# Optimization experiments

Measured on AMD Instinct MI355X. Metric: run time of the kernel, lower is better.

Reference implementation:

```python
import jax, jax.numpy as jnp
import numpy as np

B, NV, NDIRS, NRINGS, C, NF = 2, 30000, 8, 3, 16, 16


def setup_inputs() -> dict:
    key = jax.random.key(0)
    k1, k2, k3, k4, k5 = jax.random.split(key, 5)
    y = jax.random.normal(k1, (B, NV, NDIRS, C), dtype=jnp.float32)
    # sync_field: for each (batch, vertex, ring, dir) an index triple (b, v, d) into y
    v_idx = jax.random.randint(k2, (B, NV, NRINGS, NDIRS), 0, NV)
    d_idx = jax.random.randint(k3, (B, NV, NRINGS, NDIRS), 0, NDIRS)
    b_idx = jnp.broadcast_to(jnp.arange(B)[:, None, None, None], (B, NV, NRINGS, NDIRS))
    sync_field = jnp.stack([b_idx, v_idx, d_idx], axis=-1).astype(jnp.int32)
    kernel = jax.random.normal(k4, (NRINGS, NDIRS, C, NF), dtype=jnp.float32) * 0.05
    center_kernel = jax.random.normal(k5, (C, NF), dtype=jnp.float32) * 0.05
    bias = jnp.zeros((NF,), dtype=jnp.float32)
    return {"y": y, "sync_field": sync_field, "kernel": kernel,
            "center_kernel": center_kernel, "bias": bias}


def reference(y, sync_field, kernel, center_kernel, bias):
    b, nv, ndirs, c = y.shape
    nrings = kernel.shape[0]
    nf = kernel.shape[-1]
    # tf.gather_nd: index triples (batch, vertex, dir) -> channel vectors
    patches = y[sync_field[..., 0], sync_field[..., 1], sync_field[..., 2]]  # (b, nv, nrings, ndirs, c)
    patches = patches.reshape(b * nv, nrings, ndirs, c)
    # circular padding along direction axis: width becomes 2*ndirs-1
    patches = jnp.concatenate([patches, patches[:, :, :-1, :]], axis=2)
    # valid conv with (nrings, ndirs) kernel -> (b*nv, 1, ndirs, nf)
    out = jax.lax.conv_general_dilated(
        patches, kernel, window_strides=(1, 1), padding='VALID',
        dimension_numbers=('NHWC', 'HWIO', 'NHWC'))
    out = out.reshape(b, nv, ndirs, nf)
    out = out + jnp.einsum('bvdc,cf->bvdf', y, center_kernel) + bias
    out = jax.nn.relu(out)
    return jnp.max(out, axis=2)  # take_max over directions -> (b, nv, nf)
```

## Files before the change

kernel.cpp:

```cpp
#include <hip/hip_runtime.h>
#include <hip/hip_bf16.h>

static constexpr int kB = 2;
static constexpr int kNV = 30000;
static constexpr int kD = 8;
static constexpr int kR = 3;
static constexpr int kC = 16;
static constexpr int kF = 16;
static constexpr int NP = (kB * kNV) / 2;
static constexpr int S  = 4096;

typedef short short8  __attribute__((ext_vector_type(8)));
typedef float floatx4 __attribute__((ext_vector_type(4)));

static constexpr int CENT_OFS   = 1536;
static constexpr int BUF_STRIDE = 2560;

__device__ __forceinline__ unsigned pkbf16(float lo, float hi) {
    union { __hip_bfloat162 h; unsigned u; } cv;
    cv.h = __float22bfloat162_rn(make_float2(lo, hi));
    return cv.u;
}

__global__ __launch_bounds__(64, 4) void sgc_kernel(
    const float* __restrict__ y,
    const int*   __restrict__ sync_field,
    const float* __restrict__ kern,
    const float* __restrict__ ck,
    const float* __restrict__ bias,
    float*       __restrict__ out)
{
    __shared__ __align__(16) char smem[2 * BUF_STRIDE];

    const int lane = threadIdx.x;
    const int wid  = blockIdx.x;
    const int f    = lane & 15;
    const int q    = lane >> 4;
    const int mvtx = (lane >> 3) & 1;
    const int md   = lane & 7;
    const int eSub = lane >> 2;
    const int iq   = lane & 3;

    {
        const int buf = lane >> 5, z = lane & 31;
        const int ofs = buf * BUF_STRIDE + CENT_OFS + (z >> 1) * 64 + 32 + (z & 1) * 16;
        *(uint4*)(smem + ofs) = make_uint4(0u, 0u, 0u, 0u);
    }

    int aOfs[12];
    short8 bfrag[13];
#pragma unroll
    for (int kk = 0; kk < 12; ++kk) {
        const int g   = kk * 4 + q;
        const int dd  = (g * 43) >> 8;
        const int rem = g - dd * 6;
        const int r   = rem >> 1;
        const int ch  = rem & 1;
        const int rot = (md + dd) & 7;
        aOfs[kk] = ((mvtx * 3 + r) * 8 + rot) * 32 + ch * 16;
        const int be = ((r * 8 + dd) * 16 + ch * 8) * 16 + f;
        union { unsigned u[4]; short8 v; } t;
#pragma unroll
        for (int j = 0; j < 4; ++j)
            t.u[j] = pkbf16(kern[be + (2 * j) * 16], kern[be + (2 * j + 1) * 16]);
        bfrag[kk] = t.v;
    }
    {
        union { unsigned u[4]; short8 v; } t;
        if (q < 2) {
#pragma unroll
            for (int j = 0; j < 4; ++j)
                t.u[j] = pkbf16(ck[(q * 8 + 2 * j) * 16 + f],
                                ck[(q * 8 + 2 * j + 1) * 16 + f]);
        } else {
            t.u[0] = t.u[1] = t.u[2] = t.u[3] = 0u;
        }
        bfrag[12] = t.v;
    }
    const float biasv = bias[f];

    auto cl = [](int v) { return v < NP ? v : NP - 1; };

    int off[3];
    float4 A0, A1, A2, Ac, B0, B1, B2, Bc;

#define SF_PRE(cc) do { \
        const int base_ = (cc) * 48; \
        _Pragma("unroll") \
        for (int g_ = 0; g_ < 3; ++g_) { \
            const int* s_ = sync_field + (size_t)(base_ + g_ * 16 + eSub) * 3; \
            off[g_] = ((s_[0] * kNV + s_[1]) * kD + s_[2]) * 64 + iq * 16; \
        } \
    } while (0)

#define ISSUE_G(Rv, cc) do { \
        Rv##0 = *reinterpret_cast<const float4*>( \
                    reinterpret_cast<const char*>(y) + off[0]); \
        Rv##1 = *reinterpret_cast<const float4*>( \
                    reinterpret_cast<const char*>(y) + off[1]); \
        Rv##2 = *reinterpret_cast<const float4*>( \
                    reinterpret_cast<const char*>(y) + off[2]); \
        Rv##c = reinterpret_cast<const float4*>(y + (size_t)(cc) * 256)[lane]; \
    } while (0)

#define STAGE(Rv, bufbase) do { \
        const float4 g0_ = Rv##0, g1_ = Rv##1, g2_ = Rv##2, gc_ = Rv##c; \
        uint2 w_; \
        w_.x = pkbf16(g0_.x, g0_.y); w_.y = pkbf16(g0_.z, g0_.w); \
        *(uint2*)((bufbase) + 0 * 512 + lane * 8) = w_; \
        w_.x = pkbf16(g1_.x, g1_.y); w_.y = pkbf16(g1_.z, g1_.w); \
        *(uint2*)((bufbase) + 1 * 512 + lane * 8) = w_; \
        w_.x = pkbf16(g2_.x, g2_.y); w_.y = pkbf16(g2_.z, g2_.w); \
        *(uint2*)((bufbase) + 2 * 512 + lane * 8) = w_; \
        w_.x = pkbf16(gc_.x, gc_.y); w_.y = pkbf16(gc_.z, gc_.w); \
        *(uint2*)((bufbase) + CENT_OFS + eSub * 64 + iq * 8) = w_; \
    } while (0)

#define DRAIN do { \
        __asm__ __volatile__("" ::: "memory"); \
        __builtin_amdgcn_s_waitcnt(0xC07F);  \
        __asm__ __volatile__("" ::: "memory"); \
    } while (0)

#define COMPUTE_STORE(bufbase, pp) do { \
        floatx4 acc0 = { biasv, biasv, biasv, biasv }; \
        floatx4 acc1 = { 0.f, 0.f, 0.f, 0.f }; \
        _Pragma("unroll") \
        for (int kk_ = 0; kk_ < 12; kk_ += 2) { \
            const short8 a0_ = *(const short8*)((bufbase) + aOfs[kk_]); \
            const short8 a1_ = *(const short8*)((bufbase) + aOfs[kk_ + 1]); \
            acc0 = __builtin_amdgcn_mfma_f32_16x16x32_bf16(a0_, bfrag[kk_], acc0, 0, 0, 0); \
            acc1 = __builtin_amdgcn_mfma_f32_16x16x32_bf16(a1_, bfrag[kk_ + 1], acc1, 0, 0, 0); \
        } \
        { \
            const short8 ac_ = *(const short8*)((bufbase) + CENT_OFS \
                                                + (lane & 15) * 64 + q * 16); \
            acc0 = __builtin_amdgcn_mfma_f32_16x16x32_bf16(ac_, bfrag[12], acc0, 0, 0, 0); \
        } \
        float mx = fmaxf(fmaxf(acc0[0] + acc1[0], acc0[1] + acc1[1]), \
                         fmaxf(acc0[2] + acc1[2], acc0[3] + acc1[3])); \
        mx = fmaxf(mx, 0.0f); \
        mx = fmaxf(mx, __shfl_xor(mx, 16, 64)); \
        if (((lane >> 4) & 1) == 0) \
            out[(2 * (pp) + (lane >> 5)) * kF + f] = mx; \
    } while (0)

    int p = wid;
    SF_PRE(p);
    ISSUE_G(A, p);
    SF_PRE(cl(p + S));
    ISSUE_G(B, cl(p + S));
    SF_PRE(cl(p + 2 * S));
    STAGE(A, smem);
    ISSUE_G(A, cl(p + 2 * S));
    SF_PRE(cl(p + 3 * S));

    for (;;) {
        STAGE(B, smem + BUF_STRIDE);
        ISSUE_G(B, cl(p + 3 * S));
        SF_PRE(cl(p + 4 * S));
        DRAIN;
        COMPUTE_STORE(smem, p);
        p += S; if (p >= NP) break;

        STAGE(A, smem);
        ISSUE_G(A, cl(p + 3 * S));
        SF_PRE(cl(p + 4 * S));
        DRAIN;
        COMPUTE_STORE(smem + BUF_STRIDE, p);
        p += S; if (p >= NP) break;
    }

#undef SF_PRE
#undef ISSUE_G
#undef STAGE
#undef DRAIN
#undef COMPUTE_STORE
}

extern "C" void kernel_launch(void* const* d_in, const int* in_sizes, int n_in,
                              void* d_out, int out_size, void* d_ws, size_t ws_size,
                              hipStream_t stream) {
    const float* y    = reinterpret_cast<const float*>(d_in[0]);
    const int*   sf   = reinterpret_cast<const int*>(d_in[1]);
    const float* kern = reinterpret_cast<const float*>(d_in[2]);
    const float* ck   = reinterpret_cast<const float*>(d_in[3]);
    const float* bias = reinterpret_cast<const float*>(d_in[4]);
    float* out = reinterpret_cast<float*>(d_out);

    sgc_kernel<<<S, 64, 0, stream>>>(y, sf, kern, ck, bias, out);
}
```

Baseline: 131.2 us.

## Pre-convert y to a bf16 workspace table and gather bf16 in main kernel

Adds a prepass kernel that converts y from fp32 to bf16 into the workspace. The main kernel then gathers 8-byte bf16 vectors instead of 16-byte fp32 vectors, which halves the random-gather bytes and removes the per-element conversion before the LDS store. The grid size and launch bounds also change. The cost is an extra kernel launch plus a full read and write pass over y. An fp32 fallback path is kept for when the workspace is missing or too small.

```diff
diff --git a/kernel.cpp b/kernel.cpp
--- a/kernel.cpp
+++ b/kernel.cpp
@@ -8,7 +8,9 @@
 static constexpr int kC = 16;
 static constexpr int kF = 16;
 static constexpr int NP = (kB * kNV) / 2;
-static constexpr int S  = 4096;
+static constexpr int S  = 3840;
+
+static constexpr size_t WS_BYTES = (size_t)kB * kNV * kD * kC * 2;
 
 typedef short short8  __attribute__((ext_vector_type(8)));
 typedef float floatx4 __attribute__((ext_vector_type(4)));
@@ -22,12 +24,31 @@
     return cv.u;
 }
 
-__global__ __launch_bounds__(64, 4) void sgc_kernel(
+__device__ __forceinline__ uint2 to_lds8(const uint2& v) { return v; }
+__device__ __forceinline__ uint2 to_lds8(const float4& v) {
+    uint2 w; w.x = pkbf16(v.x, v.y); w.y = pkbf16(v.z, v.w); return w;
+}
+
+__global__ __launch_bounds__(256) void cvt_kernel(
+    const float* __restrict__ y, uint4* __restrict__ o)
+{
+    const int t = blockIdx.x * 256 + threadIdx.x;
+    const float4 a = reinterpret_cast<const float4*>(y)[2 * t];
+    const float4 b = reinterpret_cast<const float4*>(y)[2 * t + 1];
+    uint4 w;
+    w.x = pkbf16(a.x, a.y); w.y = pkbf16(a.z, a.w);
+    w.z = pkbf16(b.x, b.y); w.w = pkbf16(b.z, b.w);
+    o[t] = w;
+}
+
+template <bool WS16>
+__global__ __launch_bounds__(64) void sgc_kernel(
     const float* __restrict__ y,
     const int*   __restrict__ sync_field,
     const float* __restrict__ kern,
     const float* __restrict__ ck,
     const float* __restrict__ bias,
+    const char*  __restrict__ ytab,
     float*       __restrict__ out)
 {
     __shared__ __align__(16) char smem[2 * BUF_STRIDE];
@@ -40,6 +61,12 @@
     const int md   = lane & 7;
     const int eSub = lane >> 2;
     const int iq   = lane & 3;
+
+    using gvec_t = std::conditional_t<WS16, uint2, float4>;
+    constexpr int ESH   = WS16 ? 5 : 6;
+    constexpr int LSH   = WS16 ? 3 : 4;
+    constexpr int CENTB = WS16 ? 512 : 1024;
+    const char* gb = WS16 ? ytab : reinterpret_cast<const char*>(y);
 
     {
         const int buf = lane >> 5, z = lane & 31;
@@ -82,38 +109,31 @@
     auto cl = [](int v) { return v < NP ? v : NP - 1; };
 
     int off[3];
-    float4 A0, A1, A2, Ac, B0, B1, B2, Bc;
+    gvec_t A0, A1, A2, Ac, B0, B1, B2, Bc;
 
 #define SF_PRE(cc) do { \
         const int base_ = (cc) * 48; \
         _Pragma("unroll") \
         for (int g_ = 0; g_ < 3; ++g_) { \
             const int* s_ = sync_field + (size_t)(base_ + g_ * 16 + eSub) * 3; \
-            off[g_] = ((s_[0] * kNV + s_[1]) * kD + s_[2]) * 64 + iq * 16; \
+            off[g_] = (((s_[0] * kNV + s_[1]) * kD + s_[2]) << ESH) + (iq << LSH); \
         } \
     } while (0)
 
 #define ISSUE_G(Rv, cc) do { \
-        Rv##0 = *reinterpret_cast<const float4*>( \
-                    reinterpret_cast<const char*>(y) + off[0]); \
-        Rv##1 = *reinterpret_cast<const float4*>( \
-                    reinterpret_cast<const char*>(y) + off[1]); \
-        Rv##2 = *reinterpret_cast<const float4*>( \
-                    reinterpret_cast<const char*>(y) + off[2]); \
-        Rv##c = reinterpret_cast<const float4*>(y + (size_t)(cc) * 256)[lane]; \
+        Rv##0 = *reinterpret_cast<const gvec_t*>(gb + off[0]); \
+        Rv##1 = *reinterpret_cast<const gvec_t*>(gb + off[1]); \
+        Rv##2 = *reinterpret_cast<const gvec_t*>(gb + off[2]); \
+        Rv##c = *reinterpret_cast<const gvec_t*>( \
+                    gb + (size_t)(cc) * CENTB + lane * sizeof(gvec_t)); \
     } while (0)
 
 #define STAGE(Rv, bufbase) do { \
-        const float4 g0_ = Rv##0, g1_ = Rv##1, g2_ = Rv##2, gc_ = Rv##c; \
-        uint2 w_; \
-        w_.x = pkbf16(g0_.x, g0_.y); w_.y = pkbf16(g0_.z, g0_.w); \
-        *(uint2*)((bufbase) + 0 * 512 + lane * 8) = w_; \
-        w_.x = pkbf16(g1_.x, g1_.y); w_.y = pkbf16(g1_.z, g1_.w); \
-        *(uint2*)((bufbase) + 1 * 512 + lane * 8) = w_; \
-        w_.x = pkbf16(g2_.x, g2_.y); w_.y = pkbf16(g2_.z, g2_.w); \
-        *(uint2*)((bufbase) + 2 * 512 + lane * 8) = w_; \
-        w_.x = pkbf16(gc_.x, gc_.y); w_.y = pkbf16(gc_.z, gc_.w); \
-        *(uint2*)((bufbase) + CENT_OFS + eSub * 64 + iq * 8) = w_; \
+        const gvec_t g0_ = Rv##0, g1_ = Rv##1, g2_ = Rv##2, gc_ = Rv##c; \
+        *(uint2*)((bufbase) + 0 * 512 + lane * 8) = to_lds8(g0_); \
+        *(uint2*)((bufbase) + 1 * 512 + lane * 8) = to_lds8(g1_); \
+        *(uint2*)((bufbase) + 2 * 512 + lane * 8) = to_lds8(g2_); \
+        *(uint2*)((bufbase) + CENT_OFS + eSub * 64 + iq * 8) = to_lds8(gc_); \
     } while (0)
 
 #define DRAIN do { \
@@ -188,5 +208,11 @@
     const float* bias = reinterpret_cast<const float*>(d_in[4]);
     float* out = reinterpret_cast<float*>(d_out);
 
-    sgc_kernel<<<S, 64, 0, stream>>>(y, sf, kern, ck, bias, out);
-}
+    if (d_ws != nullptr && ws_size >= WS_BYTES) {
+        cvt_kernel<<<3750, 256, 0, stream>>>(y, reinterpret_cast<uint4*>(d_ws));
+        sgc_kernel<true><<<S, 64, 0, stream>>>(
+            y, sf, kern, ck, bias, reinterpret_cast<const char*>(d_ws), out);
+    } else {
+        sgc_kernel<false><<<S, 64, 0, stream>>>(y, sf, kern, ck, bias, nullptr, out);
+    }
+}
```

After: 117.3 us. 10.6% less time.
